# Optimization experiments

Hardware: AMD Instinct MI355X
Metric: run time of the kernel (lower is better)

The kernel has to match this reference:

```python
import jax, jax.numpy as jnp
import numpy as np

BS, S, D, H = 2, 2048, 1024, 16
DH = D // H  # 64


def setup_inputs() -> dict:
    key = jax.random.key(0)
    k1, k2, k3 = jax.random.split(key, 3)
    x = jax.random.normal(k1, (BS, S, D), dtype=jnp.float32)
    w_qkv = jax.random.normal(k2, (D, H, 3 * DH), dtype=jnp.float32) * (D ** -0.5)
    b_qkv = jnp.zeros((H, 3 * DH), dtype=jnp.float32)
    w_out = jax.random.normal(k3, (H, DH, D), dtype=jnp.float32) * (D ** -0.5)
    b_out = jnp.zeros((D,), dtype=jnp.float32)
    return {"x": x, "w_qkv": w_qkv, "b_qkv": b_qkv, "w_out": w_out, "b_out": b_out}


def reference(x, w_qkv, b_qkv, w_out, b_out):
    dtype = x.dtype
    # QKV projection: DenseGeneral(features=(H, 3*DH)) -> [B, S, H, 3*DH]
    qkv = jnp.einsum("bsd,dhf->bshf", x, w_qkv) + b_qkv
    q, k, v = jnp.split(qkv, 3, axis=-1)  # each [B, S, H, DH]

    scale = DH ** -0.5
    q = (q * scale).astype(jnp.float32)
    k = k.astype(jnp.float32)
    # Full causal attention with fp32 scores (as in original)
    weights = jnp.einsum("bqhd,bkhd->bhqk", q, k)  # [B, H, S, S]
    causal = jnp.tril(jnp.ones((S, S), dtype=bool))[None, None, :, :]
    weights = jnp.where(causal, weights, jnp.finfo(jnp.float32).min)
    weights = jax.nn.softmax(weights, axis=-1).astype(dtype)
    attn = jnp.einsum("bhqk,bkhd->bqhd", weights, v).astype(dtype)

    # Output projection: DenseGeneral(D, axis=(-2, -1))
    out = jnp.einsum("bqhd,hdo->bqo", attn, w_out) + b_out
    return out
```

## Files before the change

kernel.cpp:

```cpp
#include <hip/hip_runtime.h>
#include <hip/hip_bf16.h>
#include <stdint.h>

#define NBS 2
#define SEQ 2048
#define DMODEL 1024
#define NH 16
#define DHEAD 64
#define MROWS (NBS*SEQ)
#define NQKV (NH*3*DHEAD)

typedef __bf16 bf16;
typedef __bf16 bf16x8 __attribute__((ext_vector_type(8)));
typedef float f32x4 __attribute__((ext_vector_type(4)));
typedef float f32x16 __attribute__((ext_vector_type(16)));
typedef unsigned int u32x2 __attribute__((ext_vector_type(2)));

#define LOG2E 1.44269504088896f
#define QSCALE (0.125f * LOG2E)

static __device__ __forceinline__ void gload_lds16(const bf16* g, bf16* l) {
    __builtin_amdgcn_global_load_lds(
        (const __attribute__((address_space(1))) uint32_t*)g,
        (__attribute__((address_space(3))) uint32_t*)l, 16, 0, 0);
}

static __device__ __forceinline__ bf16x8 ld_b8(const bf16* p) {
    return __builtin_bit_cast(bf16x8, *(const uint4*)p);
}

static __device__ __forceinline__ uint32_t pk_bf16(float lo, float hi) {
    unsigned short l = __builtin_bit_cast(unsigned short, (bf16)lo);
    unsigned short h = __builtin_bit_cast(unsigned short, (bf16)hi);
    return ((uint32_t)h << 16) | (uint32_t)l;
}

static __device__ __forceinline__ u32x2 lane_swap32(uint32_t a, uint32_t b, int lane) {
#if __has_builtin(__builtin_amdgcn_permlane32_swap)
    return __builtin_amdgcn_permlane32_swap(a, b, false, false);
#else
    uint32_t sa = __shfl_xor(a, 32), sb = __shfl_xor(b, 32);
    u32x2 r;
    r.x = (lane >= 32) ? sb : a;
    r.y = (lane >= 32) ? b : sa;
    return r;
#endif
}


__global__ void k_cvt(const float* __restrict__ in, bf16* __restrict__ out, int n4) {
    int i = blockIdx.x * blockDim.x + threadIdx.x;
    if (i < n4) {
        float4 v = ((const float4*)in)[i];
        ushort4 o;
        o.x = __builtin_bit_cast(unsigned short, (bf16)v.x);
        o.y = __builtin_bit_cast(unsigned short, (bf16)v.y);
        o.z = __builtin_bit_cast(unsigned short, (bf16)v.z);
        o.w = __builtin_bit_cast(unsigned short, (bf16)v.w);
        ((ushort4*)out)[i] = o;
    }
}

__global__ void k_tcvt(const float* __restrict__ in, bf16* __restrict__ out, int R, int C) {
    __shared__ float t[32][33];
    int tx = threadIdx.x, ty = threadIdx.y;
    int r0 = blockIdx.y * 32, c0 = blockIdx.x * 32;
#pragma unroll
    for (int i = 0; i < 4; i++)
        t[ty + i*8][tx] = in[(size_t)(r0 + ty + i*8) * C + (c0 + tx)];
    __syncthreads();
#pragma unroll
    for (int i = 0; i < 4; i++)
        out[(size_t)(c0 + ty + i*8) * R + (r0 + tx)] = (bf16)t[tx][ty + i*8];
}

template<int KD>
static __device__ __forceinline__ void gemm_tile(
        const bf16* __restrict__ A, const bf16* __restrict__ Bt,
        bf16* As, bf16* Bs, f32x4 acc[4][4], int tile_m, int tile_n) {
    int tid = threadIdx.x;
    int wave = tid >> 6, lane = tid & 63;
    int wr = wave >> 1, wc = wave & 1;
    int g = lane >> 4, r = lane & 15;
    int srow = lane >> 2, schunk = (lane & 3) * 8;

#pragma unroll
    for (int m = 0; m < 4; m++)
#pragma unroll
        for (int n = 0; n < 4; n++)
            acc[m][n] = (f32x4){0.f, 0.f, 0.f, 0.f};

    for (int k0 = 0; k0 < KD; k0 += 32) {
#pragma unroll
        for (int i = 0; i < 2; i++) {
            int ii = wave + i * 4;
            gload_lds16(A  + (size_t)(tile_m + ii*16 + srow) * KD + k0 + schunk, As + ii*512);
            gload_lds16(Bt + (size_t)(tile_n + ii*16 + srow) * KD + k0 + schunk, Bs + ii*512);
        }
        __syncthreads();
        bf16x8 af[4], bfr[4];
#pragma unroll
        for (int m = 0; m < 4; m++) af[m]  = *(const bf16x8*)(As + (wr*64 + m*16 + r)*32 + g*8);
#pragma unroll
        for (int n = 0; n < 4; n++) bfr[n] = *(const bf16x8*)(Bs + (wc*64 + n*16 + r)*32 + g*8);
#pragma unroll
        for (int m = 0; m < 4; m++)
#pragma unroll
            for (int n = 0; n < 4; n++)
                acc[m][n] = __builtin_amdgcn_mfma_f32_16x16x32_bf16(af[m], bfr[n], acc[m][n], 0, 0, 0);
        __syncthreads();
    }
}

__global__ __launch_bounds__(256) void k_gemm_qkv(
        const bf16* __restrict__ A, const bf16* __restrict__ Bt,
        const float* __restrict__ bias,
        bf16* __restrict__ Q, bf16* __restrict__ Kp, bf16* __restrict__ Vp) {
    __shared__ __align__(16) bf16 As[128*32];
    __shared__ __align__(16) bf16 Bs[128*32];
    f32x4 acc[4][4];
    int tile_m = blockIdx.y * 128, tile_n = blockIdx.x * 128;
    gemm_tile<DMODEL>(A, Bt, As, Bs, acc, tile_m, tile_n);

    int wave = threadIdx.x >> 6, lane = threadIdx.x & 63;
    int wr = wave >> 1, wc = wave & 1, g = lane >> 4, r = lane & 15;
#pragma unroll
    for (int m = 0; m < 4; m++) {
#pragma unroll
        for (int n = 0; n < 4; n++) {
            int col = tile_n + wc*64 + n*16 + r;
            int h = col / 192, f = col % 192;
            int kind = f >> 6, d = f & 63;
            float bv = bias[col];
#pragma unroll
            for (int j = 0; j < 4; j++) {
                int row = tile_m + wr*64 + m*16 + g*4 + j;
                int b = row >> 11, s = row & 2047;
                float v = acc[m][n][j] + bv;
                size_t addr = (((size_t)(b*NH + h)) * SEQ + s) * DHEAD + d;
                if (kind == 0)      Q[addr]  = (bf16)(v * QSCALE);
                else if (kind == 1) Kp[addr] = (bf16)v;
                else                Vp[addr] = (bf16)v;
            }
        }
    }
}

__global__ __launch_bounds__(256) void k_gemm_out(
        const bf16* __restrict__ A, const bf16* __restrict__ Bt,
        const float* __restrict__ bias, float* __restrict__ out) {
    __shared__ __align__(16) bf16 As[128*32];
    __shared__ __align__(16) bf16 Bs[128*32];
    f32x4 acc[4][4];
    int tile_m = blockIdx.y * 128, tile_n = blockIdx.x * 128;
    gemm_tile<DMODEL>(A, Bt, As, Bs, acc, tile_m, tile_n);

    int wave = threadIdx.x >> 6, lane = threadIdx.x & 63;
    int wr = wave >> 1, wc = wave & 1, g = lane >> 4, r = lane & 15;
#pragma unroll
    for (int m = 0; m < 4; m++) {
#pragma unroll
        for (int n = 0; n < 4; n++) {
            int col = tile_n + wc*64 + n*16 + r;
            float bv = bias[col];
#pragma unroll
            for (int j = 0; j < 4; j++) {
                int row = tile_m + wr*64 + m*16 + g*4 + j;
                out[(size_t)row * DMODEL + col] = acc[m][n][j] + bv;
            }
        }
    }
}

#define QBLK 128
#define KVB 64

__global__ __launch_bounds__(256) void k_attn(
        const bf16* __restrict__ Q, const bf16* __restrict__ K,
        const bf16* __restrict__ V, bf16* __restrict__ O) {
    int bh = blockIdx.y;
    int qc = (bh >= 16) ? (15 - blockIdx.x) : blockIdx.x;
    int q0 = qc * QBLK;
    int tid = threadIdx.x, wave = tid >> 6, lane = tid & 63;
    int l31 = lane & 31, hi = lane >> 5;

    __shared__ __align__(16) bf16 Ks[2][KVB*72];
    __shared__ __align__(16) bf16 VsT[2][KVB*72];

    const bf16* Kg = K + (size_t)bh * SEQ * DHEAD;
    const bf16* Vg = V + (size_t)bh * SEQ * DHEAD;

    const bf16* qrow_p = Q + ((size_t)bh * SEQ + q0 + wave*32 + l31) * DHEAD;
    bf16x8 qa2[4];
#pragma unroll
    for (int c = 0; c < 4; c++) qa2[c] = ld_b8(qrow_p + c*16 + hi*8);

    f32x16 o32[2];
    const f32x16 z16 = {0,0,0,0,0,0,0,0,0,0,0,0,0,0,0,0};
    o32[0] = z16; o32[1] = z16;
    float l_part = 0.f;

    int nt = 2*qc + 2;
    int qrow = q0 + wave*32 + l31;
    int qmax_wave = q0 + wave*32 + 31;
    int qmin_wave = q0 + wave*32;

    int krow0 = tid >> 3, kseg0 = (tid & 7) * 8;
    int krow1 = (tid + 256) >> 3, kseg1 = (tid & 7) * 8;
    int vrow = tid & 63, vd0 = (tid >> 6) * 8, vd1 = ((tid >> 6) + 4) * 8;

    bf16x8 kreg[2], vreg[2];
    kreg[0] = ld_b8(Kg + (size_t)krow0 * DHEAD + kseg0);
    kreg[1] = ld_b8(Kg + (size_t)krow1 * DHEAD + kseg1);
    vreg[0] = ld_b8(Vg + (size_t)vrow * DHEAD + vd0);
    vreg[1] = ld_b8(Vg + (size_t)vrow * DHEAD + vd1);

    int cur = 0;
    for (int t = 0; t < nt; t++) {
        int kv0 = t * KVB;
        *(uint4*)&Ks[cur][krow0*72 + kseg0] = __builtin_bit_cast(uint4, kreg[0]);
        *(uint4*)&Ks[cur][krow1*72 + kseg1] = __builtin_bit_cast(uint4, kreg[1]);
#pragma unroll
        for (int j = 0; j < 8; j++) VsT[cur][(vd0 + j)*72 + vrow] = vreg[0][j];
#pragma unroll
        for (int j = 0; j < 8; j++) VsT[cur][(vd1 + j)*72 + vrow] = vreg[1][j];
        __syncthreads();

        if (t + 1 < nt) {
            int kv1 = kv0 + KVB;
            kreg[0] = ld_b8(Kg + (size_t)(kv1 + krow0) * DHEAD + kseg0);
            kreg[1] = ld_b8(Kg + (size_t)(kv1 + krow1) * DHEAD + kseg1);
            vreg[0] = ld_b8(Vg + (size_t)(kv1 + vrow) * DHEAD + vd0);
            vreg[1] = ld_b8(Vg + (size_t)(kv1 + vrow) * DHEAD + vd1);
        }

        if (kv0 <= qmax_wave) {
            f32x16 st[2];
            st[0] = z16; st[1] = z16;
#pragma unroll
            for (int c = 0; c < 4; c++) {
#pragma unroll
                for (int rb = 0; rb < 2; rb++) {
                    bf16x8 kf = ld_b8(&Ks[cur][(rb*32 + l31)*72 + c*16 + hi*8]);
                    st[rb] = __builtin_amdgcn_mfma_f32_32x32x16_bf16(kf, qa2[c], st[rb], 0, 0, 0);
                }
            }
            bool needm = (kv0 + KVB - 1) > qmin_wave;
            float l_add = 0.f;
#pragma unroll
            for (int rb = 0; rb < 2; rb++) {
#pragma unroll
                for (int reg = 0; reg < 16; reg++) {
                    float e = __builtin_amdgcn_exp2f(st[rb][reg]);
                    if (needm) {
                        int kv = kv0 + rb*32 + (reg & 3) + 8*(reg >> 2) + 4*hi;
                        if (kv > qrow) e = 0.f;
                    }
                    l_add += e;
                    st[rb][reg] = e;
                }
            }
            l_part += l_add;

            bf16x8 pa[4];
#pragma unroll
            for (int c = 0; c < 4; c++) {
                const f32x16& pp = st[c >> 1];
                const int base = (c & 1) * 8;
                uint32_t a0 = pk_bf16(pp[base+0], pp[base+1]);
                uint32_t a1 = pk_bf16(pp[base+2], pp[base+3]);
                uint32_t b0 = pk_bf16(pp[base+4], pp[base+5]);
                uint32_t b1 = pk_bf16(pp[base+6], pp[base+7]);
                u32x2 s0 = lane_swap32(a0, b0, lane);
                u32x2 s1 = lane_swap32(a1, b1, lane);
                uint4 fr = {s0.x, s1.x, s0.y, s1.y};
                pa[c] = __builtin_bit_cast(bf16x8, fr);
            }

#pragma unroll
            for (int dblk = 0; dblk < 2; dblk++) {
#pragma unroll
                for (int c = 0; c < 4; c++) {
                    bf16x8 vf = ld_b8(&VsT[cur][(dblk*32 + l31)*72 + c*16 + hi*8]);
                    o32[dblk] = __builtin_amdgcn_mfma_f32_32x32x16_bf16(pa[c], vf, o32[dblk], 0, 0, 0);
                }
            }
        }
        cur ^= 1;
    }

    l_part += __shfl_xor(l_part, 32);
    float linv = 1.0f / l_part;

    float lrv[16];
#pragma unroll
    for (int reg = 0; reg < 16; reg++) {
        int qr = (reg & 3) + 8*(reg >> 2) + 4*hi;
        lrv[reg] = __shfl(linv, qr);
    }

    int b = bh >> 4, h = bh & 15;
#pragma unroll
    for (int reg = 0; reg < 16; reg++) {
        int qr = (reg & 3) + 8*(reg >> 2) + 4*hi;
        int srow = q0 + wave*32 + qr;
        size_t base = (((size_t)b * SEQ + srow) * NH + h) * DHEAD + l31;
        O[base]      = (bf16)(o32[0][reg] * lrv[reg]);
        O[base + 32] = (bf16)(o32[1][reg] * lrv[reg]);
    }
}


extern "C" void kernel_launch(void* const* d_in, const int* in_sizes, int n_in,
                              void* d_out, int out_size, void* d_ws, size_t ws_size,
                              hipStream_t stream) {
    const float* x     = (const float*)d_in[0];
    const float* w_qkv = (const float*)d_in[1];
    const float* b_qkv = (const float*)d_in[2];
    const float* w_out = (const float*)d_in[3];
    const float* b_out = (const float*)d_in[4];
    float* out = (float*)d_out;

    char* ws = (char*)d_ws;
    bf16* xb   = (bf16*)(ws);
    bf16* wqkT = (bf16*)(ws + 8388608);
    bf16* woT  = (bf16*)(ws + 14680064);
    bf16* qb   = (bf16*)(ws + 16777216);
    bf16* kb   = (bf16*)(ws + 25165824);
    bf16* vb   = (bf16*)(ws + 33554432);
    bf16* attn = xb;

    k_cvt<<<(MROWS*DMODEL/4 + 255)/256, 256, 0, stream>>>(x, xb, MROWS*DMODEL/4);
    dim3 tb(32, 8);
    k_tcvt<<<dim3(NQKV/32, DMODEL/32), tb, 0, stream>>>(w_qkv, wqkT, DMODEL, NQKV);
    k_tcvt<<<dim3(DMODEL/32, DMODEL/32), tb, 0, stream>>>(w_out, woT, DMODEL, DMODEL);

    k_gemm_qkv<<<dim3(NQKV/128, MROWS/128), 256, 0, stream>>>(xb, wqkT, b_qkv, qb, kb, vb);
    k_attn<<<dim3(SEQ/QBLK, NBS*NH), 256, 0, stream>>>(qb, kb, vb, attn);
    k_gemm_out<<<dim3(DMODEL/128, MROWS/128), 256, 0, stream>>>(attn, woT, b_out, out);
}
```

Before: 124.7 us.

## Store V transposed from QKV GEMM and drop LDS staging in attention

The QKV projection epilogue now writes V in a transposed [bh, d, s] layout. The attention kernel no longer stages K and V through double-buffered shared memory with block-wide barriers. Each wave loads its K and V^T MFMA fragments straight from global memory (relying on cache) and runs only as many KV tiles as its own causal range needs. This removes LDS writes, the scalar transpose stores and the __syncthreads calls. The cost is redundant global/L2 traffic across the four waves, no explicit prefetch overlap, and strided scalar stores for V^T in the GEMM epilogue.

```diff
diff --git a/kernel.cpp b/kernel.cpp
--- a/kernel.cpp
+++ b/kernel.cpp
@@ -115,7 +115,7 @@
 __global__ __launch_bounds__(256) void k_gemm_qkv(
         const bf16* __restrict__ A, const bf16* __restrict__ Bt,
         const float* __restrict__ bias,
-        bf16* __restrict__ Q, bf16* __restrict__ Kp, bf16* __restrict__ Vp) {
+        bf16* __restrict__ Q, bf16* __restrict__ Kp, bf16* __restrict__ Vt) {
     __shared__ __align__(16) bf16 As[128*32];
     __shared__ __align__(16) bf16 Bs[128*32];
     f32x4 acc[4][4];
@@ -137,10 +137,13 @@
                 int row = tile_m + wr*64 + m*16 + g*4 + j;
                 int b = row >> 11, s = row & 2047;
                 float v = acc[m][n][j] + bv;
-                size_t addr = (((size_t)(b*NH + h)) * SEQ + s) * DHEAD + d;
-                if (kind == 0)      Q[addr]  = (bf16)(v * QSCALE);
-                else if (kind == 1) Kp[addr] = (bf16)v;
-                else                Vp[addr] = (bf16)v;
+                if (kind == 0) {
+                    Q[(((size_t)(b*NH + h)) * SEQ + s) * DHEAD + d] = (bf16)(v * QSCALE);
+                } else if (kind == 1) {
+                    Kp[(((size_t)(b*NH + h)) * SEQ + s) * DHEAD + d] = (bf16)v;
+                } else {
+                    Vt[(((size_t)(b*NH + h)) * DHEAD + d) * SEQ + s] = (bf16)v;
+                }
             }
         }
     }
@@ -177,116 +180,89 @@
 
 __global__ __launch_bounds__(256) void k_attn(
         const bf16* __restrict__ Q, const bf16* __restrict__ K,
-        const bf16* __restrict__ V, bf16* __restrict__ O) {
+        const bf16* __restrict__ Vt, bf16* __restrict__ O) {
     int bh = blockIdx.y;
-    int qc = (bh >= 16) ? (15 - blockIdx.x) : blockIdx.x;
+    int qc = (bh >= 16) ? (15 - (int)blockIdx.x) : (int)blockIdx.x;
     int q0 = qc * QBLK;
     int tid = threadIdx.x, wave = tid >> 6, lane = tid & 63;
     int l31 = lane & 31, hi = lane >> 5;
 
-    __shared__ __align__(16) bf16 Ks[2][KVB*72];
-    __shared__ __align__(16) bf16 VsT[2][KVB*72];
-
-    const bf16* Kg = K + (size_t)bh * SEQ * DHEAD;
-    const bf16* Vg = V + (size_t)bh * SEQ * DHEAD;
-
-    const bf16* qrow_p = Q + ((size_t)bh * SEQ + q0 + wave*32 + l31) * DHEAD;
+    const bf16* Kg = K  + (size_t)bh * SEQ * DHEAD;
+    const bf16* Vg = Vt + (size_t)bh * DHEAD * SEQ;
+
+    int qb = q0 + wave * 32;
+    int qrow = qb + l31;
+
+    const bf16* qrow_p = Q + ((size_t)bh * SEQ + qrow) * DHEAD;
     bf16x8 qa2[4];
 #pragma unroll
     for (int c = 0; c < 4; c++) qa2[c] = ld_b8(qrow_p + c*16 + hi*8);
 
+    const f32x16 z16 = {0,0,0,0,0,0,0,0,0,0,0,0,0,0,0,0};
     f32x16 o32[2];
-    const f32x16 z16 = {0,0,0,0,0,0,0,0,0,0,0,0,0,0,0,0};
     o32[0] = z16; o32[1] = z16;
     float l_part = 0.f;
 
-    int nt = 2*qc + 2;
-    int qrow = q0 + wave*32 + l31;
-    int qmax_wave = q0 + wave*32 + 31;
-    int qmin_wave = q0 + wave*32;
-
-    int krow0 = tid >> 3, kseg0 = (tid & 7) * 8;
-    int krow1 = (tid + 256) >> 3, kseg1 = (tid & 7) * 8;
-    int vrow = tid & 63, vd0 = (tid >> 6) * 8, vd1 = ((tid >> 6) + 4) * 8;
-
-    bf16x8 kreg[2], vreg[2];
-    kreg[0] = ld_b8(Kg + (size_t)krow0 * DHEAD + kseg0);
-    kreg[1] = ld_b8(Kg + (size_t)krow1 * DHEAD + kseg1);
-    vreg[0] = ld_b8(Vg + (size_t)vrow * DHEAD + vd0);
-    vreg[1] = ld_b8(Vg + (size_t)vrow * DHEAD + vd1);
-
-    int cur = 0;
+    int nt = ((qb + 31) >> 6) + 1;
+
     for (int t = 0; t < nt; t++) {
-        int kv0 = t * KVB;
-        *(uint4*)&Ks[cur][krow0*72 + kseg0] = __builtin_bit_cast(uint4, kreg[0]);
-        *(uint4*)&Ks[cur][krow1*72 + kseg1] = __builtin_bit_cast(uint4, kreg[1]);
-#pragma unroll
-        for (int j = 0; j < 8; j++) VsT[cur][(vd0 + j)*72 + vrow] = vreg[0][j];
-#pragma unroll
-        for (int j = 0; j < 8; j++) VsT[cur][(vd1 + j)*72 + vrow] = vreg[1][j];
-        __syncthreads();
-
-        if (t + 1 < nt) {
-            int kv1 = kv0 + KVB;
-            kreg[0] = ld_b8(Kg + (size_t)(kv1 + krow0) * DHEAD + kseg0);
-            kreg[1] = ld_b8(Kg + (size_t)(kv1 + krow1) * DHEAD + kseg1);
-            vreg[0] = ld_b8(Vg + (size_t)(kv1 + vrow) * DHEAD + vd0);
-            vreg[1] = ld_b8(Vg + (size_t)(kv1 + vrow) * DHEAD + vd1);
-        }
-
-        if (kv0 <= qmax_wave) {
-            f32x16 st[2];
-            st[0] = z16; st[1] = z16;
-#pragma unroll
-            for (int c = 0; c < 4; c++) {
-#pragma unroll
-                for (int rb = 0; rb < 2; rb++) {
-                    bf16x8 kf = ld_b8(&Ks[cur][(rb*32 + l31)*72 + c*16 + hi*8]);
-                    st[rb] = __builtin_amdgcn_mfma_f32_32x32x16_bf16(kf, qa2[c], st[rb], 0, 0, 0);
+        int kv0 = t << 6;
+
+        f32x16 st[2];
+        st[0] = z16; st[1] = z16;
+#pragma unroll
+        for (int c = 0; c < 4; c++) {
+#pragma unroll
+            for (int rb = 0; rb < 2; rb++) {
+                bf16x8 kf = ld_b8(Kg + (size_t)(kv0 + rb*32 + l31) * DHEAD + c*16 + hi*8);
+                st[rb] = __builtin_amdgcn_mfma_f32_32x32x16_bf16(kf, qa2[c], st[rb], 0, 0, 0);
+            }
+        }
+
+        bf16x8 vf[2][4];
+#pragma unroll
+        for (int dblk = 0; dblk < 2; dblk++)
+#pragma unroll
+            for (int c = 0; c < 4; c++)
+                vf[dblk][c] = ld_b8(Vg + (size_t)(dblk*32 + l31) * SEQ + kv0 + c*16 + hi*8);
+
+        bool needm = (kv0 + KVB - 1) > qb;
+        float l_add = 0.f;
+#pragma unroll
+        for (int rb = 0; rb < 2; rb++) {
+#pragma unroll
+            for (int reg = 0; reg < 16; reg++) {
+                float e = __builtin_amdgcn_exp2f(st[rb][reg]);
+                if (needm) {
+                    int kv = kv0 + rb*32 + (reg & 3) + 8*(reg >> 2) + 4*hi;
+                    if (kv > qrow) e = 0.f;
                 }
+                l_add += e;
+                st[rb][reg] = e;
             }
-            bool needm = (kv0 + KVB - 1) > qmin_wave;
-            float l_add = 0.f;
-#pragma unroll
-            for (int rb = 0; rb < 2; rb++) {
-#pragma unroll
-                for (int reg = 0; reg < 16; reg++) {
-                    float e = __builtin_amdgcn_exp2f(st[rb][reg]);
-                    if (needm) {
-                        int kv = kv0 + rb*32 + (reg & 3) + 8*(reg >> 2) + 4*hi;
-                        if (kv > qrow) e = 0.f;
-                    }
-                    l_add += e;
-                    st[rb][reg] = e;
-                }
-            }
-            l_part += l_add;
-
-            bf16x8 pa[4];
-#pragma unroll
-            for (int c = 0; c < 4; c++) {
-                const f32x16& pp = st[c >> 1];
-                const int base = (c & 1) * 8;
-                uint32_t a0 = pk_bf16(pp[base+0], pp[base+1]);
-                uint32_t a1 = pk_bf16(pp[base+2], pp[base+3]);
-                uint32_t b0 = pk_bf16(pp[base+4], pp[base+5]);
-                uint32_t b1 = pk_bf16(pp[base+6], pp[base+7]);
-                u32x2 s0 = lane_swap32(a0, b0, lane);
-                u32x2 s1 = lane_swap32(a1, b1, lane);
-                uint4 fr = {s0.x, s1.x, s0.y, s1.y};
-                pa[c] = __builtin_bit_cast(bf16x8, fr);
-            }
-
-#pragma unroll
-            for (int dblk = 0; dblk < 2; dblk++) {
-#pragma unroll
-                for (int c = 0; c < 4; c++) {
-                    bf16x8 vf = ld_b8(&VsT[cur][(dblk*32 + l31)*72 + c*16 + hi*8]);
-                    o32[dblk] = __builtin_amdgcn_mfma_f32_32x32x16_bf16(pa[c], vf, o32[dblk], 0, 0, 0);
-                }
-            }
-        }
-        cur ^= 1;
+        }
+        l_part += l_add;
+
+        bf16x8 pa[4];
+#pragma unroll
+        for (int c = 0; c < 4; c++) {
+            const f32x16& pp = st[c >> 1];
+            const int base = (c & 1) * 8;
+            uint32_t a0 = pk_bf16(pp[base+0], pp[base+1]);
+            uint32_t a1 = pk_bf16(pp[base+2], pp[base+3]);
+            uint32_t b0 = pk_bf16(pp[base+4], pp[base+5]);
+            uint32_t b1 = pk_bf16(pp[base+6], pp[base+7]);
+            u32x2 s0 = lane_swap32(a0, b0, lane);
+            u32x2 s1 = lane_swap32(a1, b1, lane);
+            uint4 fr = {s0.x, s1.x, s0.y, s1.y};
+            pa[c] = __builtin_bit_cast(bf16x8, fr);
+        }
+
+#pragma unroll
+        for (int dblk = 0; dblk < 2; dblk++)
+#pragma unroll
+            for (int c = 0; c < 4; c++)
+                o32[dblk] = __builtin_amdgcn_mfma_f32_32x32x16_bf16(pa[c], vf[dblk][c], o32[dblk], 0, 0, 0);
     }
 
     l_part += __shfl_xor(l_part, 32);
```

Measured after the change: 156.4 us. 25.5% more time.
